# Kernel optimization log

Measured on AMD Instinct MI355X. Metric: run time of the kernel, lower is better.

Reference implementation:

```python
import jax, jax.numpy as jnp
import numpy as np

D, L, DIM, G = 64, 64, 512, 256      # dialogues, utterances/dialogue, feat dim, graph dim
TOPK_FRAC = 0.2
TAU = 0.07


def setup_inputs() -> dict:
    key = jax.random.key(0)
    ks = jax.random.split(key, 7)
    N = D * L
    t = jax.random.normal(ks[0], (N, DIM), dtype=jnp.float32)
    a = jax.random.normal(ks[1], (N, DIM), dtype=jnp.float32)
    v = jax.random.normal(ks[2], (N, DIM), dtype=jnp.float32)
    W_fc = jax.random.normal(ks[3], (DIM, G), dtype=jnp.float32) / np.sqrt(DIM)
    b_fc = jnp.zeros((G,), dtype=jnp.float32)
    W_h = jax.random.normal(ks[4], (G, G), dtype=jnp.float32) / np.sqrt(G)
    b_h = jnp.zeros((G,), dtype=jnp.float32)
    dia_len = np.full((D,), L, dtype=np.int64)  # uniform dialogue lengths
    return {"t": t, "a": a, "v": v, "W_fc": W_fc, "b_fc": b_fc,
            "W_h": W_h, "b_h": b_h, "dia_len": dia_len}


def _contrastive_loss(x, y, tau=TAU):
    # symmetric InfoNCE with matched-index positives
    xn = x / (jnp.linalg.norm(x, axis=-1, keepdims=True) + 1e-8)
    yn = y / (jnp.linalg.norm(y, axis=-1, keepdims=True) + 1e-8)
    sim = (xn @ yn.T) / tau                     # [N, N]
    pos_xy = jnp.diagonal(jax.nn.log_softmax(sim, axis=1))
    pos_yx = jnp.diagonal(jax.nn.log_softmax(sim, axis=0))
    return -(pos_xy.mean() + pos_yx.mean()) / 2.0


def _forward(t, a, v, W_fc, b_fc, W_h, b_h, dia_len):
    dl = np.asarray(dia_len)
    d, l = dl.shape[0], int(dl[0])              # uniform lengths assumed
    m = 3 * l                                   # nodes (and hyperedges) per dialogue
    k = int(l * TOPK_FRAC)
    dim = t.shape[-1]

    # per-dialogue node features in original order [t_i; a_i; v_i]
    feat = jnp.concatenate([t.reshape(d, l, dim),
                            a.reshape(d, l, dim),
                            v.reshape(d, l, dim)], axis=1)   # [d, m, dim]

    # squared euclidean distances (same ordering as torch.cdist for top-k smallest)
    sq = jnp.sum(feat * feat, axis=-1)                        # [d, m]
    d2 = sq[:, :, None] + sq[:, None, :] - 2.0 * jnp.einsum('dmf,dnf->dmn', feat, feat)
    d2 = jax.lax.stop_gradient(jnp.maximum(d2, 0.0))
    _, idx = jax.lax.top_k(-d2, k)                            # [d, m, k] nearest nodes

    # boolean incidence H[d, e, n] = node n participates in hyperedge e
    # (set-union dedup in the original == boolean OR here)
    node_ids = jnp.arange(m)
    H_nb = (idx[..., None] == node_ids).any(axis=2)           # [d, m, m]
    u = node_ids // 3                                         # central utterance of edge j
    cent = ((node_ids[None, :] == u[:, None]) |
            (node_ids[None, :] == u[:, None] + l) |
            (node_ids[None, :] == u[:, None] + 2 * l))        # [m, m]
    H = (H_nb | cent[None]).astype(feat.dtype)                # [d, m, m]

    # fc projection
    X = feat @ W_fc + b_fc                                    # [d, m, G]

    # hypergraph conv: node -> hyperedge (mean) -> node (mean), then Linear+ReLU
    deg_e = H.sum(axis=2, keepdims=True)                      # [d, m, 1]
    E = jnp.einsum('den,dng->deg', H, X) / deg_e              # edge features
    deg_v = H.sum(axis=1)[..., None]                          # [d, m, 1]
    Y = jnp.einsum('den,deg->dng', H, E) / deg_v              # node features
    out = jax.nn.relu(Y @ W_h + b_h)                          # [d, m, G]

    # reverse_features: regroup by modality across dialogues
    tn = out[:, :l].reshape(d * l, -1)
    an = out[:, l:2 * l].reshape(d * l, -1)
    vn = out[:, 2 * l:].reshape(d * l, -1)
    out_cat = jnp.concatenate([tn, an, vn], axis=1)           # [N, 3G]

    loss = (_contrastive_loss(tn, an) + _contrastive_loss(tn, vn)
            + _contrastive_loss(an, vn)) / 3.0
    return out_cat, loss


def reference(t, a, v, W_fc, b_fc, W_h, b_h, dia_len):
    return _forward(t, a, v, W_fc, b_fc, W_h, b_h, dia_len)
```

## Files before the change

kernel.cpp:

```cpp
#include <hip/hip_runtime.h>
#include <math.h>

#define NDIAL 64
#define M3    192
#define DIMF  512
#define GDIM  256
#define NROW  4096
#define TOPK  12
#define INV_TAU (1.0f/0.07f)

typedef __attribute__((ext_vector_type(8))) short bf16x8;
typedef __attribute__((ext_vector_type(4))) float f32x4;
typedef __attribute__((ext_vector_type(8))) ushort us8;
typedef _Float16 f16x8 __attribute__((ext_vector_type(8)));
typedef _Float16 f16x4v __attribute__((ext_vector_type(4)));
typedef __attribute__((address_space(3))) ushort lds_us;
typedef const __attribute__((address_space(1))) ushort gm_us;

__device__ __forceinline__ ushort f2bf(float f) {
    unsigned u = __float_as_uint(f);
    unsigned r = (u + 0x7fff + ((u >> 16) & 1)) >> 16;
    return (ushort)r;
}

__global__ void kprep(const float* __restrict__ t, const float* __restrict__ a,
                      const float* __restrict__ v, const float* __restrict__ Wfc,
                      const float* __restrict__ Wh, _Float16* __restrict__ featb,
                      _Float16* __restrict__ featlo, _Float16* __restrict__ WfcT,
                      _Float16* __restrict__ WhT,
                      float* __restrict__ sq, float* __restrict__ rs,
                      float* __restrict__ cs, float* __restrict__ degV,
                      _Float16* __restrict__ HbT) {
    int b = blockIdx.x, tid = threadIdx.x;
    if (b < 6144) {
        __shared__ float part[4];
        int e = (b * 256 + tid) * 4;
        int d = e / (M3 * DIMF);
        int rem = e % (M3 * DIMF);
        int n = rem / DIMF, kk = rem % DIMF;
        int mod = n >> 6, i = n & 63;
        const float* src = ((mod == 0) ? t : (mod == 1) ? a : v)
                           + (size_t)(d * 64 + i) * DIMF + kk;
        float4 x = *(const float4*)src;
        _Float16 h0 = (_Float16)x.x, h1 = (_Float16)x.y;
        _Float16 h2 = (_Float16)x.z, h3 = (_Float16)x.w;
        f16x4v o = {h0, h1, h2, h3};
        *(f16x4v*)&featb[e] = o;
        f16x4v ol = {(_Float16)(x.x - (float)h0), (_Float16)(x.y - (float)h1),
                     (_Float16)(x.z - (float)h2), (_Float16)(x.w - (float)h3)};
        *(f16x4v*)&featlo[e] = ol;
        float s = x.x * x.x + x.y * x.y + x.z * x.z + x.w * x.w;
#pragma unroll
        for (int o2 = 32; o2; o2 >>= 1) s += __shfl_down(s, o2);
        int wv = tid >> 6;
        if ((tid & 63) == 0) part[wv] = s;
        __syncthreads();
        if (tid < 2) sq[2 * b + tid] = part[2 * tid] + part[2 * tid + 1];
    } else if (b < 6272) {
        int e = ((b - 6144) * 256 + tid) * 4;
        int g = e >> 9, kk = e & 511;
        f16x4v o = {(_Float16)Wfc[(size_t)(kk + 0) * GDIM + g],
                    (_Float16)Wfc[(size_t)(kk + 1) * GDIM + g],
                    (_Float16)Wfc[(size_t)(kk + 2) * GDIM + g],
                    (_Float16)Wfc[(size_t)(kk + 3) * GDIM + g]};
        *(f16x4v*)&WfcT[(size_t)g * DIMF + kk] = o;
    } else if (b < 6336) {
        int e = ((b - 6272) * 256 + tid) * 4;
        int go = e >> 8, g = e & 255;
        f16x4v o = {(_Float16)Wh[(size_t)(g + 0) * GDIM + go],
                    (_Float16)Wh[(size_t)(g + 1) * GDIM + go],
                    (_Float16)Wh[(size_t)(g + 2) * GDIM + go],
                    (_Float16)Wh[(size_t)(g + 3) * GDIM + go]};
        *(f16x4v*)&WhT[(size_t)go * GDIM + g] = o;
    } else if (b < 6384) {
        int i = (b - 6336) * 256 + tid;
        rs[i] = 0.f; cs[i] = 0.f; degV[i] = 0.f;
    } else {
        int i = (b - 6384) * 256 + tid;
        ulonglong2 z = {0ull, 0ull};
        *(ulonglong2*)&HbT[(size_t)i * 8] = z;
    }
}

__global__ __launch_bounds__(256) void k1_d2(const _Float16* __restrict__ featb,
                      const _Float16* __restrict__ featlo,
                      const float* __restrict__ sq,
                      float* __restrict__ d2) {
    int tileid = blockIdx.x;
    int d = blockIdx.y;
    int bi = (tileid < 3) ? 0 : (tileid < 5) ? 1 : 2;
    int bj = (tileid < 3) ? tileid : (tileid < 5) ? tileid - 2 : 2;
    const size_t base = (size_t)d * M3 * DIMF;
    const _Float16* Ah = featb  + base + (size_t)bi * 64 * DIMF;
    const _Float16* Al = featlo + base + (size_t)bi * 64 * DIMF;
    const _Float16* Bh = featb  + base + (size_t)bj * 64 * DIMF;
    const _Float16* Bl = featlo + base + (size_t)bj * 64 * DIMF;

    __shared__ __align__(16) _Float16 Ahs[64 * 40], Als[64 * 40];
    __shared__ __align__(16) _Float16 Bhs[64 * 40], Bls[64 * 40];
    const int tid = threadIdx.x;
    const int lane = tid & 63, w = tid >> 6;
    const int qd = lane >> 4, l15 = lane & 15;

    f32x4 acc[4];
#pragma unroll
    for (int fm = 0; fm < 4; fm++) acc[fm] = (f32x4){0.f, 0.f, 0.f, 0.f};

    for (int k0 = 0; k0 < DIMF; k0 += 32) {
        int row = tid >> 2, c8 = tid & 3;
        *(float4*)&Ahs[row * 40 + c8 * 8] = *(const float4*)&Ah[(size_t)row * DIMF + k0 + c8 * 8];
        *(float4*)&Als[row * 40 + c8 * 8] = *(const float4*)&Al[(size_t)row * DIMF + k0 + c8 * 8];
        *(float4*)&Bhs[row * 40 + c8 * 8] = *(const float4*)&Bh[(size_t)row * DIMF + k0 + c8 * 8];
        *(float4*)&Bls[row * 40 + c8 * 8] = *(const float4*)&Bl[(size_t)row * DIMF + k0 + c8 * 8];
        __syncthreads();
        f16x8 bh = *(const f16x8*)&Bhs[(w * 16 + l15) * 40 + qd * 8];
        f16x8 bl = *(const f16x8*)&Bls[(w * 16 + l15) * 40 + qd * 8];
#pragma unroll
        for (int fm = 0; fm < 4; fm++) {
            f16x8 ah = *(const f16x8*)&Ahs[(fm * 16 + l15) * 40 + qd * 8];
            f16x8 al = *(const f16x8*)&Als[(fm * 16 + l15) * 40 + qd * 8];
            acc[fm] = __builtin_amdgcn_mfma_f32_16x16x32_f16(ah, bh, acc[fm], 0, 0, 0);
            acc[fm] = __builtin_amdgcn_mfma_f32_16x16x32_f16(ah, bl, acc[fm], 0, 0, 0);
            acc[fm] = __builtin_amdgcn_mfma_f32_16x16x32_f16(al, bh, acc[fm], 0, 0, 0);
            acc[fm] = __builtin_amdgcn_mfma_f32_16x16x32_f16(al, bl, acc[fm], 0, 0, 0);
        }
        __syncthreads();
    }

    const float* sqd = sq + d * M3;
    float* outp = d2 + (size_t)d * M3 * M3;
#pragma unroll
    for (int fm = 0; fm < 4; fm++)
#pragma unroll
        for (int rg = 0; rg < 4; rg++) {
            int il = bi * 64 + fm * 16 + qd * 4 + rg;
            int jl = bj * 64 + w * 16 + l15;
            float vv = fmaxf(sqd[il] + sqd[jl] - 2.f * acc[fm][rg], 0.f);
            outp[(size_t)il * M3 + jl] = vv;
            if (bi != bj) outp[(size_t)jl * M3 + il] = vv;
        }
}

__global__ void k2_topk(const float* __restrict__ d2, _Float16* __restrict__ Hb,
                        _Float16* __restrict__ HbT, float* __restrict__ degE,
                        float* __restrict__ degV) {
    int lane = threadIdx.x & 63, wv = threadIdx.x >> 6;
    int r = blockIdx.x * 4 + wv;
    int d = r / M3, e = r % M3;
    const float* row = d2 + (size_t)r * M3;
    float w0 = row[lane], w1 = row[lane + 64], w2 = row[lane + 128];
    bool s0 = false, s1 = false, s2 = false;
#pragma unroll
    for (int it = 0; it < TOPK; it++) {
        float bv = w0; int bi = lane;
        if (w1 < bv) { bv = w1; bi = lane + 64; }
        if (w2 < bv) { bv = w2; bi = lane + 128; }
#pragma unroll
        for (int o = 1; o < 64; o <<= 1) {
            float ov = __shfl_xor(bv, o);
            int   oi = __shfl_xor(bi, o);
            if (ov < bv || (ov == bv && oi < bi)) { bv = ov; bi = oi; }
        }
        if (bi == lane)            { s0 = true; w0 = 3.4e38f; }
        else if (bi == lane + 64)  { s1 = true; w1 = 3.4e38f; }
        else if (bi == lane + 128) { s2 = true; w2 = 3.4e38f; }
    }
    int u = e / 3;
    if (lane == u) { s0 = true; s1 = true; s2 = true; }
    float f0 = s0 ? 1.f : 0.f, f1 = s1 ? 1.f : 0.f, f2 = s2 ? 1.f : 0.f;
    _Float16* Hrow = Hb + (size_t)r * M3;
    Hrow[lane] = (_Float16)f0;
    Hrow[lane + 64] = (_Float16)f1;
    Hrow[lane + 128] = (_Float16)f2;
    float cnt = f0 + f1 + f2;
#pragma unroll
    for (int o = 1; o < 64; o <<= 1) cnt += __shfl_xor(cnt, o);
    if (lane == 0) degE[r] = cnt;
    float* dv = degV + d * M3;
    _Float16* HT = HbT + (size_t)d * M3 * M3;
    if (s0) { atomicAdd(&dv[lane], 1.f);       HT[(size_t)lane * M3 + e] = (_Float16)1.f; }
    if (s1) { atomicAdd(&dv[lane + 64], 1.f);  HT[(size_t)(lane + 64) * M3 + e] = (_Float16)1.f; }
    if (s2) { atomicAdd(&dv[lane + 128], 1.f); HT[(size_t)(lane + 128) * M3 + e] = (_Float16)1.f; }
}

__global__ __launch_bounds__(192) void k34_XE(const _Float16* __restrict__ WfcT,
                      const _Float16* __restrict__ featb,
                      const float* __restrict__ bfc,
                      const _Float16* __restrict__ Hb,
                      const float* __restrict__ degE,
                      _Float16* __restrict__ ET) {
    int gb = blockIdx.x, d = blockIdx.y;
    const _Float16* A = WfcT + (size_t)gb * 32 * DIMF;
    const _Float16* B = featb + (size_t)d * M3 * DIMF;
    const _Float16* H = Hb + (size_t)d * M3 * M3;

    __shared__ __align__(16) _Float16 As[32 * 40];
    __shared__ __align__(16) _Float16 Bs[M3 * 40];
    __shared__ __align__(16) _Float16 Xls[32 * 200];
    const int tid = threadIdx.x;
    const int lane = tid & 63, w = tid >> 6;
    const int qd = lane >> 4, l15 = lane & 15;

    f32x4 acc[2][4];
#pragma unroll
    for (int fm = 0; fm < 2; fm++)
#pragma unroll
        for (int fn = 0; fn < 4; fn++) acc[fm][fn] = (f32x4){0.f, 0.f, 0.f, 0.f};

    for (int k0 = 0; k0 < DIMF; k0 += 32) {
        if (tid < 128) {
            int row = tid >> 2, c8 = tid & 3;
            *(float4*)&As[row * 40 + c8 * 8] =
                *(const float4*)&A[(size_t)row * DIMF + k0 + c8 * 8];
        }
#pragma unroll
        for (int i = 0; i < 4; i++) {
            int f = tid + i * 192;
            int row = f >> 2, c8 = f & 3;
            *(float4*)&Bs[row * 40 + c8 * 8] =
                *(const float4*)&B[(size_t)row * DIMF + k0 + c8 * 8];
        }
        __syncthreads();
        f16x8 af[2], bfr[4];
#pragma unroll
        for (int fm = 0; fm < 2; fm++)
            af[fm] = *(const f16x8*)&As[(fm * 16 + l15) * 40 + qd * 8];
#pragma unroll
        for (int fn = 0; fn < 4; fn++)
            bfr[fn] = *(const f16x8*)&Bs[(w * 64 + fn * 16 + l15) * 40 + qd * 8];
#pragma unroll
        for (int fm = 0; fm < 2; fm++)
#pragma unroll
            for (int fn = 0; fn < 4; fn++)
                acc[fm][fn] = __builtin_amdgcn_mfma_f32_16x16x32_f16(
                    af[fm], bfr[fn], acc[fm][fn], 0, 0, 0);
        __syncthreads();
    }
#pragma unroll
    for (int fm = 0; fm < 2; fm++)
#pragma unroll
        for (int rg = 0; rg < 4; rg++) {
            int row = fm * 16 + qd * 4 + rg;
            float bias = bfc[gb * 32 + row];
#pragma unroll
            for (int fn = 0; fn < 4; fn++) {
                int col = w * 64 + fn * 16 + l15;
                Xls[row * 200 + col] = (_Float16)(acc[fm][fn][rg] + bias);
            }
        }
    __syncthreads();

#pragma unroll
    for (int fm = 0; fm < 2; fm++)
#pragma unroll
        for (int fn = 0; fn < 4; fn++) acc[fm][fn] = (f32x4){0.f, 0.f, 0.f, 0.f};
    for (int k0 = 0; k0 < M3; k0 += 32) {
#pragma unroll
        for (int i = 0; i < 4; i++) {
            int f = tid + i * 192;
            int row = f >> 2, c8 = f & 3;
            *(float4*)&Bs[row * 40 + c8 * 8] =
                *(const float4*)&H[(size_t)row * M3 + k0 + c8 * 8];
        }
        __syncthreads();
        f16x8 af[2], bfr[4];
#pragma unroll
        for (int fm = 0; fm < 2; fm++)
            af[fm] = *(const f16x8*)&Xls[(fm * 16 + l15) * 200 + k0 + qd * 8];
#pragma unroll
        for (int fn = 0; fn < 4; fn++)
            bfr[fn] = *(const f16x8*)&Bs[(w * 64 + fn * 16 + l15) * 40 + qd * 8];
#pragma unroll
        for (int fm = 0; fm < 2; fm++)
#pragma unroll
            for (int fn = 0; fn < 4; fn++)
                acc[fm][fn] = __builtin_amdgcn_mfma_f32_16x16x32_f16(
                    af[fm], bfr[fn], acc[fm][fn], 0, 0, 0);
        __syncthreads();
    }
    float ide[4];
#pragma unroll
    for (int fn = 0; fn < 4; fn++)
        ide[fn] = 1.f / degE[d * M3 + w * 64 + fn * 16 + l15];
    _Float16* out = ET + (size_t)d * GDIM * M3;
#pragma unroll
    for (int fm = 0; fm < 2; fm++)
#pragma unroll
        for (int rg = 0; rg < 4; rg++) {
            int g = gb * 32 + fm * 16 + qd * 4 + rg;
#pragma unroll
            for (int fn = 0; fn < 4; fn++) {
                int e = w * 64 + fn * 16 + l15;
                out[(size_t)g * M3 + e] = (_Float16)(acc[fm][fn][rg] * ide[fn]);
            }
        }
}

__global__ __launch_bounds__(256) void k56_Yout(const _Float16* __restrict__ HbT,
                      const _Float16* __restrict__ ET,
                      const float* __restrict__ degV,
                      const _Float16* __restrict__ WhT,
                      const float* __restrict__ bh,
                      float* __restrict__ outp,
                      ushort* __restrict__ xnb) {
    int nb = blockIdx.x, d = blockIdx.y;
    int mod = nb >> 1, half = nb & 1;
    const int nlo = mod * 64 + half * 32;
    const _Float16* A = HbT + (size_t)d * M3 * M3 + (size_t)nlo * M3;
    const _Float16* B = ET + (size_t)d * GDIM * M3;

    __shared__ __align__(16) _Float16 As[32 * 40];
    __shared__ __align__(16) _Float16 Bs[GDIM * 40];
    __shared__ __align__(16) _Float16 Yls[32 * 264];
    __shared__ float tile[32 * 256];
    __shared__ float ssq[32];
    const int tid = threadIdx.x;
    const int lane = tid & 63, w = tid >> 6;
    const int qd = lane >> 4, l15 = lane & 15;
    if (tid < 32) ssq[tid] = 0.f;

    f32x4 acc[2][4];
#pragma unroll
    for (int fm = 0; fm < 2; fm++)
#pragma unroll
        for (int fn = 0; fn < 4; fn++) acc[fm][fn] = (f32x4){0.f, 0.f, 0.f, 0.f};

    for (int k0 = 0; k0 < M3; k0 += 32) {
        if (tid < 128) {
            int row = tid >> 2, c8 = tid & 3;
            *(float4*)&As[row * 40 + c8 * 8] =
                *(const float4*)&A[(size_t)row * M3 + k0 + c8 * 8];
        }
#pragma unroll
        for (int i = 0; i < 4; i++) {
            int f = tid + i * 256;
            int row = f >> 2, c8 = f & 3;
            *(float4*)&Bs[row * 40 + c8 * 8] =
                *(const float4*)&B[(size_t)row * M3 + k0 + c8 * 8];
        }
        __syncthreads();
        f16x8 af[2], bfr[4];
#pragma unroll
        for (int fm = 0; fm < 2; fm++)
            af[fm] = *(const f16x8*)&As[(fm * 16 + l15) * 40 + qd * 8];
#pragma unroll
        for (int fn = 0; fn < 4; fn++)
            bfr[fn] = *(const f16x8*)&Bs[(w * 64 + fn * 16 + l15) * 40 + qd * 8];
#pragma unroll
        for (int fm = 0; fm < 2; fm++)
#pragma unroll
            for (int fn = 0; fn < 4; fn++)
                acc[fm][fn] = __builtin_amdgcn_mfma_f32_16x16x32_f16(
                    af[fm], bfr[fn], acc[fm][fn], 0, 0, 0);
        __syncthreads();
    }
#pragma unroll
    for (int fm = 0; fm < 2; fm++)
#pragma unroll
        for (int rg = 0; rg < 4; rg++) {
            int ml = fm * 16 + qd * 4 + rg;
            float idv = 1.f / degV[d * M3 + nlo + ml];
#pragma unroll
            for (int fn = 0; fn < 4; fn++) {
                int g = w * 64 + fn * 16 + l15;
                Yls[ml * 264 + g] = (_Float16)(acc[fm][fn][rg] * idv);
            }
        }
    __syncthreads();

#pragma unroll
    for (int fm = 0; fm < 2; fm++)
#pragma unroll
        for (int fn = 0; fn < 4; fn++) acc[fm][fn] = (f32x4){0.f, 0.f, 0.f, 0.f};
    for (int k0 = 0; k0 < GDIM; k0 += 32) {
#pragma unroll
        for (int i = 0; i < 4; i++) {
            int f = tid + i * 256;
            int row = f >> 2, c8 = f & 3;
            *(float4*)&Bs[row * 40 + c8 * 8] =
                *(const float4*)&WhT[(size_t)row * GDIM + k0 + c8 * 8];
        }
        __syncthreads();
        f16x8 af[2], bfr[4];
#pragma unroll
        for (int fm = 0; fm < 2; fm++)
            af[fm] = *(const f16x8*)&Yls[(fm * 16 + l15) * 264 + k0 + qd * 8];
#pragma unroll
        for (int fn = 0; fn < 4; fn++)
            bfr[fn] = *(const f16x8*)&Bs[(w * 64 + fn * 16 + l15) * 40 + qd * 8];
#pragma unroll
        for (int fm = 0; fm < 2; fm++)
#pragma unroll
            for (int fn = 0; fn < 4; fn++)
                acc[fm][fn] = __builtin_amdgcn_mfma_f32_16x16x32_f16(
                    af[fm], bfr[fn], acc[fm][fn], 0, 0, 0);
        __syncthreads();
    }

    float bb[4];
#pragma unroll
    for (int fn = 0; fn < 4; fn++)
        bb[fn] = bh[w * 64 + fn * 16 + l15];
#pragma unroll
    for (int fm = 0; fm < 2; fm++)
#pragma unroll
        for (int rg = 0; rg < 4; rg++) {
            int i = fm * 16 + qd * 4 + rg;
            float* orow = outp + (size_t)(d * 64 + half * 32 + i) * 768 + mod * GDIM;
            float s2 = 0.f;
#pragma unroll
            for (int fn = 0; fn < 4; fn++) {
                int go = w * 64 + fn * 16 + l15;
                float vv = fmaxf(acc[fm][fn][rg] + bb[fn], 0.f);
                orow[go] = vv;
                tile[i * 256 + go] = vv;
                s2 += vv * vv;
            }
            s2 += __shfl_xor(s2, 1);
            s2 += __shfl_xor(s2, 2);
            s2 += __shfl_xor(s2, 4);
            s2 += __shfl_xor(s2, 8);
            if (l15 == 0) atomicAdd(&ssq[i], s2);
        }
    __syncthreads();
    if (tid < 32) ssq[tid] = 1.f / (sqrtf(ssq[tid]) + 1e-8f);
    __syncthreads();
#pragma unroll
    for (int it = 0; it < 4; it++) {
        int f = tid + it * 256;
        int row = f >> 5, c = f & 31;
        float4 xa = *(const float4*)&tile[row * 256 + c * 8];
        float4 xb = *(const float4*)&tile[row * 256 + c * 8 + 4];
        float iv = ssq[row];
        us8 o = {f2bf(xa.x * iv), f2bf(xa.y * iv), f2bf(xa.z * iv), f2bf(xa.w * iv),
                 f2bf(xb.x * iv), f2bf(xb.y * iv), f2bf(xb.z * iv), f2bf(xb.w * iv)};
        int rx = d * 64 + half * 32 + row;
        int slot = (c & 24) | ((c & 7) ^ (row & 7));
        *(us8*)&xnb[((size_t)mod * NROW + rx) * GDIM + slot * 8] = o;
    }
}

#define TILE9 128
#define STAGE9(ELT)                                                        \
    {                                                                      \
        __builtin_amdgcn_global_load_lds(pa0 + (ELT), la0, 16, 0, 0);      \
        __builtin_amdgcn_global_load_lds(pb0 + (ELT), lb0, 16, 0, 0);      \
        __builtin_amdgcn_global_load_lds(pa1 + (ELT), la1, 16, 0, 0);      \
        __builtin_amdgcn_global_load_lds(pb1 + (ELT), lb1, 16, 0, 0);      \
        __builtin_amdgcn_global_load_lds(pa2 + (ELT), la2, 16, 0, 0);      \
        __builtin_amdgcn_global_load_lds(pb2 + (ELT), lb2, 16, 0, 0);      \
        __builtin_amdgcn_global_load_lds(pa3 + (ELT), la3, 16, 0, 0);      \
        __builtin_amdgcn_global_load_lds(pb3 + (ELT), lb3, 16, 0, 0);      \
    }
__global__ __launch_bounds__(256, 4) void k9_mfma(const ushort* __restrict__ xnb,
                                                  float* __restrict__ rs,
                                                  float* __restrict__ cs,
                                                  float* __restrict__ diag) {
    int lin = blockIdx.x + (blockIdx.y << 5) + (blockIdx.z << 10);
    int vid = (lin >> 3) + (lin & 7) * 384;
    int p  = vid >> 10;
    int r0 = vid & 1023;
    int ci = r0 >> 5, cj = r0 & 31;
    int px = (p == 2) ? 1 : 0;
    int py = (p == 0) ? 1 : 2;
    const ushort* A = xnb + ((size_t)px * NROW + ci * TILE9) * GDIM;
    const ushort* B = xnb + ((size_t)py * NROW + cj * TILE9) * GDIM;

    __shared__ __align__(16) ushort As[TILE9 * 64];
    __shared__ __align__(16) ushort Bs[TILE9 * 64];

    const int tid = threadIdx.x;
    const int lane = tid & 63, w = tid >> 6;
    const int wrow = w >> 1, wcol = w & 1;
    const int qd = lane >> 4, l15 = lane & 15;
    const int lrow = lane >> 3, lslot = lane & 7;

    const int rbase = w * 32 + lrow;
    const int cbase = lslot * 8;
    const gm_us* pa0 = (gm_us*)(A + (size_t)(rbase +  0) * GDIM + cbase);
    const gm_us* pa1 = (gm_us*)(A + (size_t)(rbase +  8) * GDIM + cbase);
    const gm_us* pa2 = (gm_us*)(A + (size_t)(rbase + 16) * GDIM + cbase);
    const gm_us* pa3 = (gm_us*)(A + (size_t)(rbase + 24) * GDIM + cbase);
    const gm_us* pb0 = (gm_us*)(B + (size_t)(rbase +  0) * GDIM + cbase);
    const gm_us* pb1 = (gm_us*)(B + (size_t)(rbase +  8) * GDIM + cbase);
    const gm_us* pb2 = (gm_us*)(B + (size_t)(rbase + 16) * GDIM + cbase);
    const gm_us* pb3 = (gm_us*)(B + (size_t)(rbase + 24) * GDIM + cbase);
    lds_us* la0 = (lds_us*)&As[(w * 32 +  0) * 64];
    lds_us* la1 = (lds_us*)&As[(w * 32 +  8) * 64];
    lds_us* la2 = (lds_us*)&As[(w * 32 + 16) * 64];
    lds_us* la3 = (lds_us*)&As[(w * 32 + 24) * 64];
    lds_us* lb0 = (lds_us*)&Bs[(w * 32 +  0) * 64];
    lds_us* lb1 = (lds_us*)&Bs[(w * 32 +  8) * 64];
    lds_us* lb2 = (lds_us*)&Bs[(w * 32 + 16) * 64];
    lds_us* lb3 = (lds_us*)&Bs[(w * 32 + 24) * 64];

    f32x4 acc[4][4] = {};

    auto compute = [&]() {
#pragma unroll
        for (int kk = 0; kk < 2; kk++) {
            bf16x8 af[4], bfv[4];
#pragma unroll
            for (int fm = 0; fm < 4; fm++) {
                int ar = wrow * 64 + fm * 16 + l15;
                af[fm] = *(const bf16x8*)&As[ar * 64 + ((kk * 4 + qd) ^ (ar & 7)) * 8];
            }
#pragma unroll
            for (int fn = 0; fn < 4; fn++) {
                int br = wcol * 64 + fn * 16 + l15;
                bfv[fn] = *(const bf16x8*)&Bs[br * 64 + ((kk * 4 + qd) ^ (br & 7)) * 8];
            }
#pragma unroll
            for (int fm = 0; fm < 4; fm++)
#pragma unroll
                for (int fn = 0; fn < 4; fn++)
                    acc[fm][fn] = __builtin_amdgcn_mfma_f32_16x16x32_bf16(
                        af[fm], bfv[fn], acc[fm][fn], 0, 0, 0);
        }
    };

    STAGE9(0);   __syncthreads(); compute(); __syncthreads();
    STAGE9(64);  __syncthreads(); compute(); __syncthreads();
    STAGE9(128); __syncthreads(); compute(); __syncthreads();
    STAGE9(192); __syncthreads(); compute(); __syncthreads();

    const float C2 = INV_TAU * 1.44269504088896f;
    f32x4 rv[4] = {};
    f32x4 cv[4] = {};
#pragma unroll
    for (int fm = 0; fm < 4; fm++)
#pragma unroll
        for (int fn = 0; fn < 4; fn++) {
            f32x4 sv = acc[fm][fn] * C2;
            f32x4 ev;
#pragma unroll
            for (int rg = 0; rg < 4; rg++)
                ev[rg] = exp2f(sv[rg]);
            rv[fm] += ev;
            cv[fn] += ev;
        }
    if (ci == cj) {
#pragma unroll
        for (int fm = 0; fm < 4; fm++)
#pragma unroll
            for (int fn = 0; fn < 4; fn++)
#pragma unroll
                for (int rg = 0; rg < 4; rg++) {
                    int lr = wrow * 64 + fm * 16 + qd * 4 + rg;
                    int lc = wcol * 64 + fn * 16 + l15;
                    if (lr == lc)
                        diag[p * NROW + ci * TILE9 + lr] = acc[fm][fn][rg] * INV_TAU;
                }
    }
#pragma unroll
    for (int fm = 0; fm < 4; fm++)
#pragma unroll
        for (int rg = 0; rg < 4; rg++) {
            float s = rv[fm][rg];
            s += __shfl_xor(s, 1);
            s += __shfl_xor(s, 2);
            s += __shfl_xor(s, 4);
            s += __shfl_xor(s, 8);
            if (l15 == 0)
                atomicAdd(&rs[p * NROW + ci * TILE9 + wrow * 64 + fm * 16 + qd * 4 + rg], s);
        }
#pragma unroll
    for (int fn = 0; fn < 4; fn++) {
        float s = (cv[fn][0] + cv[fn][1]) + (cv[fn][2] + cv[fn][3]);
        s += __shfl_xor(s, 16);
        s += __shfl_xor(s, 32);
        if (qd == 0)
            atomicAdd(&cs[p * NROW + cj * TILE9 + wcol * 64 + fn * 16 + l15], s);
    }
}

__global__ void k10_loss(const float* __restrict__ diag, const float* __restrict__ rs,
                         const float* __restrict__ cs, float* __restrict__ outp) {
    float acc = 0.f;
    for (int i = threadIdx.x; i < 3 * NROW; i += 256)
        acc += 2.f * diag[i] - logf(rs[i]) - logf(cs[i]);
    int lane = threadIdx.x & 63, wv = threadIdx.x >> 6;
    for (int o = 32; o; o >>= 1) acc += __shfl_down(acc, o);
    __shared__ float red[4];
    if (lane == 0) red[wv] = acc;
    __syncthreads();
    if (threadIdx.x == 0) {
        float tot = red[0] + red[1] + red[2] + red[3];
        outp[(size_t)NROW * 768] = -tot / (NROW * 6.0f);
    }
}

extern "C" void kernel_launch(void* const* d_in, const int* in_sizes, int n_in,
                              void* d_out, int out_size, void* d_ws, size_t ws_size,
                              hipStream_t stream) {
    const float* t   = (const float*)d_in[0];
    const float* a   = (const float*)d_in[1];
    const float* v   = (const float*)d_in[2];
    const float* Wfc = (const float*)d_in[3];
    const float* bfc = (const float*)d_in[4];
    const float* Wh  = (const float*)d_in[5];
    const float* bh  = (const float*)d_in[6];
    float* outp = (float*)d_out;
    float* ws = (float*)d_ws;

    float* sq    = ws;
    float* d2    = sq + 12288;
    float* HbF   = d2 + 2359296;
    float* HbTF  = HbF + 1179648;
    float* degE  = HbTF + 1179648;
    float* degV  = degE + 12288;
    float* featF = degV + 12288;
    float* WfcTF = featF + 3145728;
    float* WhTF  = WfcTF + 65536;
    float* XTF   = WhTF + 32768;
    float* ETF   = XTF + 1572864;
    float* YF    = ETF + 1572864;
    float* rs    = YF + 1572864;
    float* cs    = rs + 12288;
    float* diag  = cs + 12288;

    _Float16* Hb    = (_Float16*)HbF;
    _Float16* HbT   = (_Float16*)HbTF;
    _Float16* featb = (_Float16*)featF;
    _Float16* WfcT  = (_Float16*)WfcTF;
    _Float16* WhT   = (_Float16*)WhTF;
    _Float16* ET    = (_Float16*)ETF;
    ushort*   xnb   = (ushort*)d2;
    _Float16* featlo = (_Float16*)XTF;

    kprep  <<<7536, 256, 0, stream>>>(t, a, v, Wfc, Wh, featb, featlo, WfcT,
                                      WhT, sq, rs, cs, degV, HbT);
    k1_d2  <<<dim3(6, 64), 256, 0, stream>>>(featb, featlo, sq, d2);
    k2_topk<<<3072, 256, 0, stream>>>(d2, Hb, HbT, degE, degV);
    k34_XE <<<dim3(8, 64), 192, 0, stream>>>(WfcT, featb, bfc, Hb, degE, ET);
    k56_Yout<<<dim3(6, 64), 256, 0, stream>>>(HbT, ET, degV, WhT, bh, outp, xnb);
    k9_mfma<<<dim3(32, 32, 3), 256, 0, stream>>>(xnb, rs, cs, diag);
    k10_loss<<<1, 256, 0, stream>>>(diag, rs, cs, outp);
}
```

Measured before the change: 251.9 us.

## Fuse fp16 conversion into Gram and XE kernels, merge prep with distance kernel

Drops the separate featb/featlo fp16 staging buffers. The Gram-matrix tile loop now converts fp32 inputs to hi/lo fp16 on the fly, and that work runs as extra blocks inside the prep kernel, removing one launch. The distance finalization (sq terms and clamp) moves into the top-k kernel, so the Gram blocks do not depend on the sq reduction running concurrently. k34_XE also reads fp32 inputs and converts them directly. This saves global writes and reads of the fp16 copies, but the fp32 loads read twice as many bytes and conversion work is repeated across tiles.

```diff
diff --git a/kernel.cpp b/kernel.cpp
--- a/kernel.cpp
+++ b/kernel.cpp
@@ -23,18 +23,105 @@
     return (ushort)r;
 }
 
-__global__ void kprep(const float* __restrict__ t, const float* __restrict__ a,
-                      const float* __restrict__ v, const float* __restrict__ Wfc,
-                      const float* __restrict__ Wh, _Float16* __restrict__ featb,
-                      _Float16* __restrict__ featlo, _Float16* __restrict__ WfcT,
-                      _Float16* __restrict__ WhT,
+__device__ __forceinline__ const float* node_ptr(const float* t, const float* a,
+                                                 const float* v, int d, int j) {
+    int mod = j >> 6, i = j & 63;
+    const float* base = (mod == 0) ? t : (mod == 1) ? a : v;
+    return base + (size_t)(d * 64 + i) * DIMF;
+}
+
+__device__ __forceinline__ void cvt_hilo(const float* __restrict__ src,
+                                         f16x8* h, f16x8* l) {
+    float4 x0 = *(const float4*)src;
+    float4 x1 = *(const float4*)(src + 4);
+    f16x8 hh, ll;
+    hh[0] = (_Float16)x0.x; ll[0] = (_Float16)(x0.x - (float)hh[0]);
+    hh[1] = (_Float16)x0.y; ll[1] = (_Float16)(x0.y - (float)hh[1]);
+    hh[2] = (_Float16)x0.z; ll[2] = (_Float16)(x0.z - (float)hh[2]);
+    hh[3] = (_Float16)x0.w; ll[3] = (_Float16)(x0.w - (float)hh[3]);
+    hh[4] = (_Float16)x1.x; ll[4] = (_Float16)(x1.x - (float)hh[4]);
+    hh[5] = (_Float16)x1.y; ll[5] = (_Float16)(x1.y - (float)hh[5]);
+    hh[6] = (_Float16)x1.z; ll[6] = (_Float16)(x1.z - (float)hh[6]);
+    hh[7] = (_Float16)x1.w; ll[7] = (_Float16)(x1.w - (float)hh[7]);
+    *h = hh; *l = ll;
+}
+
+__device__ __forceinline__ f16x8 cvt_hi(const float* __restrict__ src) {
+    float4 x0 = *(const float4*)src;
+    float4 x1 = *(const float4*)(src + 4);
+    f16x8 hh;
+    hh[0] = (_Float16)x0.x; hh[1] = (_Float16)x0.y;
+    hh[2] = (_Float16)x0.z; hh[3] = (_Float16)x0.w;
+    hh[4] = (_Float16)x1.x; hh[5] = (_Float16)x1.y;
+    hh[6] = (_Float16)x1.z; hh[7] = (_Float16)x1.w;
+    return hh;
+}
+
+__global__ __launch_bounds__(256) void kA(const float* __restrict__ t,
+                      const float* __restrict__ a, const float* __restrict__ v,
+                      const float* __restrict__ Wfc, const float* __restrict__ Wh,
+                      _Float16* __restrict__ WfcT, _Float16* __restrict__ WhT,
                       float* __restrict__ sq, float* __restrict__ rs,
                       float* __restrict__ cs, float* __restrict__ degV,
-                      _Float16* __restrict__ HbT) {
+                      _Float16* __restrict__ HbT, float* __restrict__ d2) {
+    __shared__ __align__(16) _Float16 Ahs[64 * 40], Als[64 * 40];
+    __shared__ __align__(16) _Float16 Bhs[64 * 40], Bls[64 * 40];
+    __shared__ float part[4];
     int b = blockIdx.x, tid = threadIdx.x;
-    if (b < 6144) {
-        __shared__ float part[4];
-        int e = (b * 256 + tid) * 4;
+
+    if (b < 384) {
+        int tileid = b % 6;
+        int d = b / 6;
+        int bi = (tileid < 3) ? 0 : (tileid < 5) ? 1 : 2;
+        int bj = (tileid < 3) ? tileid : (tileid < 5) ? tileid - 2 : 2;
+        const float* Abase = ((bi == 0) ? t : (bi == 1) ? a : v) + (size_t)d * 64 * DIMF;
+        const float* Bbase = ((bj == 0) ? t : (bj == 1) ? a : v) + (size_t)d * 64 * DIMF;
+
+        const int lane = tid & 63, w = tid >> 6;
+        const int qd = lane >> 4, l15 = lane & 15;
+
+        f32x4 acc[4];
+#pragma unroll
+        for (int fm = 0; fm < 4; fm++) acc[fm] = (f32x4){0.f, 0.f, 0.f, 0.f};
+
+        const int row = tid >> 2, c8 = tid & 3;
+        for (int k0 = 0; k0 < DIMF; k0 += 32) {
+            f16x8 h, l;
+            cvt_hilo(&Abase[(size_t)row * DIMF + k0 + c8 * 8], &h, &l);
+            *(f16x8*)&Ahs[row * 40 + c8 * 8] = h;
+            *(f16x8*)&Als[row * 40 + c8 * 8] = l;
+            cvt_hilo(&Bbase[(size_t)row * DIMF + k0 + c8 * 8], &h, &l);
+            *(f16x8*)&Bhs[row * 40 + c8 * 8] = h;
+            *(f16x8*)&Bls[row * 40 + c8 * 8] = l;
+            __syncthreads();
+            f16x8 bh = *(const f16x8*)&Bhs[(w * 16 + l15) * 40 + qd * 8];
+            f16x8 bl = *(const f16x8*)&Bls[(w * 16 + l15) * 40 + qd * 8];
+#pragma unroll
+            for (int fm = 0; fm < 4; fm++) {
+                f16x8 ah = *(const f16x8*)&Ahs[(fm * 16 + l15) * 40 + qd * 8];
+                f16x8 al = *(const f16x8*)&Als[(fm * 16 + l15) * 40 + qd * 8];
+                acc[fm] = __builtin_amdgcn_mfma_f32_16x16x32_f16(ah, bh, acc[fm], 0, 0, 0);
+                acc[fm] = __builtin_amdgcn_mfma_f32_16x16x32_f16(ah, bl, acc[fm], 0, 0, 0);
+                acc[fm] = __builtin_amdgcn_mfma_f32_16x16x32_f16(al, bh, acc[fm], 0, 0, 0);
+                acc[fm] = __builtin_amdgcn_mfma_f32_16x16x32_f16(al, bl, acc[fm], 0, 0, 0);
+            }
+            __syncthreads();
+        }
+
+        float* outp = d2 + (size_t)d * M3 * M3;
+#pragma unroll
+        for (int fm = 0; fm < 4; fm++)
+#pragma unroll
+            for (int rg = 0; rg < 4; rg++) {
+                int il = bi * 64 + fm * 16 + qd * 4 + rg;
+                int jl = bj * 64 + w * 16 + l15;
+                float s = 2.f * acc[fm][rg];
+                outp[(size_t)il * M3 + jl] = s;
+                if (bi != bj) outp[(size_t)jl * M3 + il] = s;
+            }
+    } else if (b < 6528) {
+        int bb = b - 384;
+        int e = (bb * 256 + tid) * 4;
         int d = e / (M3 * DIMF);
         int rem = e % (M3 * DIMF);
         int n = rem / DIMF, kk = rem % DIMF;
@@ -42,113 +129,52 @@
         const float* src = ((mod == 0) ? t : (mod == 1) ? a : v)
                            + (size_t)(d * 64 + i) * DIMF + kk;
         float4 x = *(const float4*)src;
-        _Float16 h0 = (_Float16)x.x, h1 = (_Float16)x.y;
-        _Float16 h2 = (_Float16)x.z, h3 = (_Float16)x.w;
-        f16x4v o = {h0, h1, h2, h3};
-        *(f16x4v*)&featb[e] = o;
-        f16x4v ol = {(_Float16)(x.x - (float)h0), (_Float16)(x.y - (float)h1),
-                     (_Float16)(x.z - (float)h2), (_Float16)(x.w - (float)h3)};
-        *(f16x4v*)&featlo[e] = ol;
         float s = x.x * x.x + x.y * x.y + x.z * x.z + x.w * x.w;
 #pragma unroll
         for (int o2 = 32; o2; o2 >>= 1) s += __shfl_down(s, o2);
         int wv = tid >> 6;
         if ((tid & 63) == 0) part[wv] = s;
         __syncthreads();
-        if (tid < 2) sq[2 * b + tid] = part[2 * tid] + part[2 * tid + 1];
-    } else if (b < 6272) {
-        int e = ((b - 6144) * 256 + tid) * 4;
+        if (tid < 2) sq[2 * bb + tid] = part[2 * tid] + part[2 * tid + 1];
+    } else if (b < 6656) {
+        int e = ((b - 6528) * 256 + tid) * 4;
         int g = e >> 9, kk = e & 511;
         f16x4v o = {(_Float16)Wfc[(size_t)(kk + 0) * GDIM + g],
                     (_Float16)Wfc[(size_t)(kk + 1) * GDIM + g],
                     (_Float16)Wfc[(size_t)(kk + 2) * GDIM + g],
                     (_Float16)Wfc[(size_t)(kk + 3) * GDIM + g]};
         *(f16x4v*)&WfcT[(size_t)g * DIMF + kk] = o;
-    } else if (b < 6336) {
-        int e = ((b - 6272) * 256 + tid) * 4;
+    } else if (b < 6720) {
+        int e = ((b - 6656) * 256 + tid) * 4;
         int go = e >> 8, g = e & 255;
         f16x4v o = {(_Float16)Wh[(size_t)(g + 0) * GDIM + go],
                     (_Float16)Wh[(size_t)(g + 1) * GDIM + go],
                     (_Float16)Wh[(size_t)(g + 2) * GDIM + go],
                     (_Float16)Wh[(size_t)(g + 3) * GDIM + go]};
         *(f16x4v*)&WhT[(size_t)go * GDIM + g] = o;
-    } else if (b < 6384) {
-        int i = (b - 6336) * 256 + tid;
+    } else if (b < 6768) {
+        int i = (b - 6720) * 256 + tid;
         rs[i] = 0.f; cs[i] = 0.f; degV[i] = 0.f;
     } else {
-        int i = (b - 6384) * 256 + tid;
+        int i = (b - 6768) * 256 + tid;
         ulonglong2 z = {0ull, 0ull};
         *(ulonglong2*)&HbT[(size_t)i * 8] = z;
     }
 }
 
-__global__ __launch_bounds__(256) void k1_d2(const _Float16* __restrict__ featb,
-                      const _Float16* __restrict__ featlo,
-                      const float* __restrict__ sq,
-                      float* __restrict__ d2) {
-    int tileid = blockIdx.x;
-    int d = blockIdx.y;
-    int bi = (tileid < 3) ? 0 : (tileid < 5) ? 1 : 2;
-    int bj = (tileid < 3) ? tileid : (tileid < 5) ? tileid - 2 : 2;
-    const size_t base = (size_t)d * M3 * DIMF;
-    const _Float16* Ah = featb  + base + (size_t)bi * 64 * DIMF;
-    const _Float16* Al = featlo + base + (size_t)bi * 64 * DIMF;
-    const _Float16* Bh = featb  + base + (size_t)bj * 64 * DIMF;
-    const _Float16* Bl = featlo + base + (size_t)bj * 64 * DIMF;
-
-    __shared__ __align__(16) _Float16 Ahs[64 * 40], Als[64 * 40];
-    __shared__ __align__(16) _Float16 Bhs[64 * 40], Bls[64 * 40];
-    const int tid = threadIdx.x;
-    const int lane = tid & 63, w = tid >> 6;
-    const int qd = lane >> 4, l15 = lane & 15;
-
-    f32x4 acc[4];
-#pragma unroll
-    for (int fm = 0; fm < 4; fm++) acc[fm] = (f32x4){0.f, 0.f, 0.f, 0.f};
-
-    for (int k0 = 0; k0 < DIMF; k0 += 32) {
-        int row = tid >> 2, c8 = tid & 3;
-        *(float4*)&Ahs[row * 40 + c8 * 8] = *(const float4*)&Ah[(size_t)row * DIMF + k0 + c8 * 8];
-        *(float4*)&Als[row * 40 + c8 * 8] = *(const float4*)&Al[(size_t)row * DIMF + k0 + c8 * 8];
-        *(float4*)&Bhs[row * 40 + c8 * 8] = *(const float4*)&Bh[(size_t)row * DIMF + k0 + c8 * 8];
-        *(float4*)&Bls[row * 40 + c8 * 8] = *(const float4*)&Bl[(size_t)row * DIMF + k0 + c8 * 8];
-        __syncthreads();
-        f16x8 bh = *(const f16x8*)&Bhs[(w * 16 + l15) * 40 + qd * 8];
-        f16x8 bl = *(const f16x8*)&Bls[(w * 16 + l15) * 40 + qd * 8];
-#pragma unroll
-        for (int fm = 0; fm < 4; fm++) {
-            f16x8 ah = *(const f16x8*)&Ahs[(fm * 16 + l15) * 40 + qd * 8];
-            f16x8 al = *(const f16x8*)&Als[(fm * 16 + l15) * 40 + qd * 8];
-            acc[fm] = __builtin_amdgcn_mfma_f32_16x16x32_f16(ah, bh, acc[fm], 0, 0, 0);
-            acc[fm] = __builtin_amdgcn_mfma_f32_16x16x32_f16(ah, bl, acc[fm], 0, 0, 0);
-            acc[fm] = __builtin_amdgcn_mfma_f32_16x16x32_f16(al, bh, acc[fm], 0, 0, 0);
-            acc[fm] = __builtin_amdgcn_mfma_f32_16x16x32_f16(al, bl, acc[fm], 0, 0, 0);
-        }
-        __syncthreads();
-    }
-
-    const float* sqd = sq + d * M3;
-    float* outp = d2 + (size_t)d * M3 * M3;
-#pragma unroll
-    for (int fm = 0; fm < 4; fm++)
-#pragma unroll
-        for (int rg = 0; rg < 4; rg++) {
-            int il = bi * 64 + fm * 16 + qd * 4 + rg;
-            int jl = bj * 64 + w * 16 + l15;
-            float vv = fmaxf(sqd[il] + sqd[jl] - 2.f * acc[fm][rg], 0.f);
-            outp[(size_t)il * M3 + jl] = vv;
-            if (bi != bj) outp[(size_t)jl * M3 + il] = vv;
-        }
-}
-
-__global__ void k2_topk(const float* __restrict__ d2, _Float16* __restrict__ Hb,
+__global__ void k2_topk(const float* __restrict__ d2, const float* __restrict__ sq,
+                        _Float16* __restrict__ Hb,
                         _Float16* __restrict__ HbT, float* __restrict__ degE,
                         float* __restrict__ degV) {
     int lane = threadIdx.x & 63, wv = threadIdx.x >> 6;
     int r = blockIdx.x * 4 + wv;
     int d = r / M3, e = r % M3;
     const float* row = d2 + (size_t)r * M3;
-    float w0 = row[lane], w1 = row[lane + 64], w2 = row[lane + 128];
+    const float* sqd = sq + d * M3;
+    float sqe = sqd[e];
+    float w0 = fmaxf(sqe + sqd[lane]       - row[lane],       0.f);
+    float w1 = fmaxf(sqe + sqd[lane + 64]  - row[lane + 64],  0.f);
+    float w2 = fmaxf(sqe + sqd[lane + 128] - row[lane + 128], 0.f);
     bool s0 = false, s1 = false, s2 = false;
 #pragma unroll
     for (int it = 0; it < TOPK; it++) {
@@ -184,14 +210,14 @@
 }
 
 __global__ __launch_bounds__(192) void k34_XE(const _Float16* __restrict__ WfcT,
-                      const _Float16* __restrict__ featb,
+                      const float* __restrict__ t, const float* __restrict__ a,
+                      const float* __restrict__ v,
                       const float* __restrict__ bfc,
                       const _Float16* __restrict__ Hb,
                       const float* __restrict__ degE,
                       _Float16* __restrict__ ET) {
     int gb = blockIdx.x, d = blockIdx.y;
     const _Float16* A = WfcT + (size_t)gb * 32 * DIMF;
-    const _Float16* B = featb + (size_t)d * M3 * DIMF;
     const _Float16* H = Hb + (size_t)d * M3 * M3;
 
     __shared__ __align__(16) _Float16 As[32 * 40];
@@ -217,8 +243,8 @@
         for (int i = 0; i < 4; i++) {
             int f = tid + i * 192;
             int row = f >> 2, c8 = f & 3;
-            *(float4*)&Bs[row * 40 + c8 * 8] =
-                *(const float4*)&B[(size_t)row * DIMF + k0 + c8 * 8];
+            const float* src = node_ptr(t, a, v, d, row) + k0 + c8 * 8;
+            *(f16x8*)&Bs[row * 40 + c8 * 8] = cvt_hi(src);
         }
         __syncthreads();
         f16x8 af[2], bfr[4];
@@ -621,18 +647,15 @@
 
     _Float16* Hb    = (_Float16*)HbF;
     _Float16* HbT   = (_Float16*)HbTF;
-    _Float16* featb = (_Float16*)featF;
     _Float16* WfcT  = (_Float16*)WfcTF;
     _Float16* WhT   = (_Float16*)WhTF;
     _Float16* ET    = (_Float16*)ETF;
     ushort*   xnb   = (ushort*)d2;
-    _Float16* featlo = (_Float16*)XTF;
-
-    kprep  <<<7536, 256, 0, stream>>>(t, a, v, Wfc, Wh, featb, featlo, WfcT,
-                                      WhT, sq, rs, cs, degV, HbT);
-    k1_d2  <<<dim3(6, 64), 256, 0, stream>>>(featb, featlo, sq, d2);
-    k2_topk<<<3072, 256, 0, stream>>>(d2, Hb, HbT, degE, degV);
-    k34_XE <<<dim3(8, 64), 192, 0, stream>>>(WfcT, featb, bfc, Hb, degE, ET);
+
+    kA     <<<7920, 256, 0, stream>>>(t, a, v, Wfc, Wh, WfcT, WhT,
+                                      sq, rs, cs, degV, HbT, d2);
+    k2_topk<<<3072, 256, 0, stream>>>(d2, sq, Hb, HbT, degE, degV);
+    k34_XE <<<dim3(8, 64), 192, 0, stream>>>(WfcT, t, a, v, bfc, Hb, degE, ET);
     k56_Yout<<<dim3(6, 64), 256, 0, stream>>>(HbT, ET, degV, WhT, bh, outp, xnb);
     k9_mfma<<<dim3(32, 32, 3), 256, 0, stream>>>(xnb, rs, cs, diag);
     k10_loss<<<1, 256, 0, stream>>>(diag, rs, cs, outp);
```

Result: no change. 253.3 us (+0.6%).
